# Optimization experiments

Hardware: AMD Instinct MI355X
Metric: run time of the kernel (lower is better)

## Reference

```python
import jax, jax.numpy as jnp
import numpy as np

N_NODES = 50000
N_EDGES = 500000
N_FEAT = 128
EMB_DIM = 1024
HIDDEN = 128
OUT_DIM = 10
VOCAB = 55049
N_GRAPHS = 64


def setup_inputs() -> dict:
    key = jax.random.key(0)
    ks = jax.random.split(key, 12)
    x = jax.random.normal(ks[0], (N_NODES, N_FEAT), dtype=jnp.float32)
    edge_weight = jax.random.uniform(ks[1], (N_EDGES,), dtype=jnp.float32)
    edge_index = jax.random.randint(ks[2], (2, N_EDGES), 0, N_NODES)
    batch = jnp.sort(jax.random.randint(ks[3], (N_NODES,), 0, N_GRAPHS))
    node_ids = jax.random.randint(ks[4], (N_NODES,), 0, VOCAB)
    emb_table = jax.random.normal(ks[5], (VOCAB, EMB_DIM), dtype=jnp.float32)
    d_in = N_FEAT + EMB_DIM
    W1 = jax.random.normal(ks[6], (d_in, HIDDEN), dtype=jnp.float32) / np.sqrt(d_in)
    b1 = jnp.zeros((HIDDEN,), dtype=jnp.float32)
    W2 = jax.random.normal(ks[7], (HIDDEN, HIDDEN), dtype=jnp.float32) / np.sqrt(HIDDEN)
    b2 = jnp.zeros((HIDDEN,), dtype=jnp.float32)
    fcW = jax.random.normal(ks[8], (HIDDEN, OUT_DIM), dtype=jnp.float32) / np.sqrt(HIDDEN)
    fcb = jnp.zeros((OUT_DIM,), dtype=jnp.float32)
    return dict(x=x, edge_weight=edge_weight, emb_table=emb_table, W1=W1, b1=b1,
                W2=W2, b2=b2, fcW=fcW, fcb=fcb,
                edge_index=edge_index, batch=batch, node_ids=node_ids)


def gcn_conv(x, edge_index, edge_weight, W, b, n_nodes):
    # PyG GCNConv: x' = D^{-1/2} (A + I) D^{-1/2} (x W) + b, self-loop weight = 1
    x = x @ W
    src, dst = edge_index[0], edge_index[1]
    loop = jnp.arange(n_nodes)
    src = jnp.concatenate([src, loop])
    dst = jnp.concatenate([dst, loop])
    ew = jnp.concatenate([edge_weight, jnp.ones((n_nodes,), x.dtype)])
    deg = jax.ops.segment_sum(ew, dst, num_segments=n_nodes)
    dinv = jnp.where(deg > 0, jax.lax.rsqrt(deg), 0.0)
    norm = dinv[src] * ew * dinv[dst]  # [E+N]
    msgs = norm[:, None] * x[src]      # [E+N, H] gather
    out = jax.ops.segment_sum(msgs, dst, num_segments=n_nodes)  # scatter-add
    return out + b


def reference(x, edge_weight, emb_table, W1, b1, W2, b2, fcW, fcb,
              edge_index, batch, node_ids):
    n = x.shape[0]
    h = jnp.concatenate([x, emb_table[node_ids]], axis=1)  # [N, F+E]
    h = jax.nn.relu(gcn_conv(h, edge_index, edge_weight, W1, b1, n))
    h = jax.nn.relu(gcn_conv(h, edge_index, edge_weight, W2, b2, n))
    # global mean pool per graph (dropout is identity in eval)
    sums = jax.ops.segment_sum(h, batch, num_segments=N_GRAPHS)
    counts = jax.ops.segment_sum(jnp.ones((n,), h.dtype), batch, num_segments=N_GRAPHS)
    pooled = sums / jnp.maximum(counts, 1.0)[:, None]
    return pooled @ fcW + fcb
```

## Files before the change

### kernel.cpp

```cpp
#include <hip/hip_runtime.h>
#include <hip/hip_bf16.h>

#define N_NODES 50000
#define N_EDGES 500000
#define N_FEAT 128
#define EMB_DIM 1024
#define HIDDEN 128
#define OUT_DIM 10
#define N_GRAPHS 64
#define NB_NODE 196

typedef __attribute__((ext_vector_type(8))) short short8;
typedef __attribute__((ext_vector_type(4))) float f32x4;

__device__ __forceinline__ unsigned short f2bf(float f) {
    unsigned int u = __float_as_uint(f);
    return (unsigned short)((u + 0x7fffu + ((u >> 16) & 1u)) >> 16);
}
__device__ __forceinline__ float bflo(unsigned int r) { return __uint_as_float(r << 16); }
__device__ __forceinline__ float bfhi(unsigned int r) { return __uint_as_float(r & 0xffff0000u); }
__device__ __forceinline__ unsigned int packbf(float lo, float hi) {
    return ((unsigned int)f2bf(hi) << 16) | f2bf(lo);
}

__global__ __launch_bounds__(256) void k_init(unsigned long long* __restrict__ dc,
                                              float* __restrict__ sums,
                                              float* __restrict__ counts) {
    int i = blockIdx.x * 256 + threadIdx.x;
    if (i < N_NODES) dc[i] = 0ULL;
    if (i < N_GRAPHS * HIDDEN) sums[i] = 0.0f;
    if (i < N_GRAPHS) counts[i] = 0.0f;
}

__global__ __launch_bounds__(256) void k_deg(const int* __restrict__ dst,
                                             const float* __restrict__ ew,
                                             unsigned long long* __restrict__ dc) {
    int e = blockIdx.x * 256 + threadIdx.x;
    if (e < N_EDGES) {
        unsigned int fx = (unsigned int)(ew[e] * 16777216.0f);
        atomicAdd(&dc[dst[e]], (1ULL << 32) | (unsigned long long)fx);
    }
}

__global__ __launch_bounds__(256) void k_scan1(const unsigned long long* __restrict__ dc,
                                               int* __restrict__ bsum) {
    __shared__ int wsum[4];
    int i = blockIdx.x * 256 + threadIdx.x;
    int v = (i < N_NODES) ? (int)((const uint2*)dc)[i].y : 0;
#pragma unroll
    for (int off = 32; off; off >>= 1) v += __shfl_down(v, off, 64);
    if ((threadIdx.x & 63) == 0) wsum[threadIdx.x >> 6] = v;
    __syncthreads();
    if (threadIdx.x == 0) bsum[blockIdx.x] = wsum[0] + wsum[1] + wsum[2] + wsum[3];
}

__global__ __launch_bounds__(256) void k_scan2(int* __restrict__ bsum) {
    __shared__ int sh[256];
    int t = threadIdx.x;
    int v = (t < NB_NODE) ? bsum[t] : 0;
    sh[t] = v;
    __syncthreads();
    for (int off = 1; off < 256; off <<= 1) {
        int add = (t >= off) ? sh[t - off] : 0;
        __syncthreads();
        sh[t] += add;
        __syncthreads();
    }
    if (t < NB_NODE) bsum[t] = sh[t] - v;
}

__global__ __launch_bounds__(256) void k_scan3(const unsigned long long* __restrict__ dc,
                                               const int* __restrict__ bofs,
                                               int* __restrict__ cursor,
                                               int* __restrict__ rowptr,
                                               float* __restrict__ dinv) {
    __shared__ int sh[256];
    const int t = threadIdx.x;
    const int i = blockIdx.x * 256 + t;
    uint2 d = (i < N_NODES) ? ((const uint2*)dc)[i] : make_uint2(0u, 0u);
    int v = (int)d.y;
    sh[t] = v;
    __syncthreads();
    for (int off = 1; off < 256; off <<= 1) {
        int add = (t >= off) ? sh[t - off] : 0;
        __syncthreads();
        sh[t] += add;
        __syncthreads();
    }
    int ex = sh[t] - v + bofs[blockIdx.x];
    if (i < N_NODES) {
        rowptr[i] = ex;
        cursor[i] = ex;
        float deg = 1.0f + (float)d.x * (1.0f / 16777216.0f);
        dinv[i] = 1.0f / sqrtf(deg);
    }
    if (i == 0) rowptr[N_NODES] = N_EDGES;
}

__global__ __launch_bounds__(256) void k_fill(const int* __restrict__ src,
                                              const int* __restrict__ dst,
                                              const float* __restrict__ ew,
                                              const float* __restrict__ dinv,
                                              int* __restrict__ cursor,
                                              int2* __restrict__ csr) {
    int e = blockIdx.x * 256 + threadIdx.x;
    if (e >= N_EDGES) return;
    int s = src[e], d = dst[e];
    int pos = atomicAdd(&cursor[d], 1);
    float norm = dinv[s] * ew[e] * dinv[d];
    csr[pos] = make_int2(s, __float_as_int(norm));
}

__device__ __forceinline__ void prep_one(const float* __restrict__ W,
                                         unsigned short* __restrict__ Wt,
                                         int K, int t) {
    int n = t & 127;
    int c = t >> 7;
    if (c * 16 >= K) return;
    short8 h0, h1;
#pragma unroll
    for (int i = 0; i < 16; i++) {
        unsigned short h = f2bf(W[(size_t)(c * 16 + i) * HIDDEN + n]);
        if (i < 8) h0[i] = (short)h;
        else       h1[i - 8] = (short)h;
    }
    size_t o = (size_t)n * K + c * 16;
    *(short8*)&Wt[o] = h0;
    *(short8*)&Wt[o + 8] = h1;
}

__global__ __launch_bounds__(256) void k_prep(const float* __restrict__ W1,
                                              unsigned short* __restrict__ Wt1,
                                              const float* __restrict__ W2,
                                              unsigned short* __restrict__ Wt2) {
    int b = blockIdx.x;
    if (b < 36) prep_one(W1, Wt1, N_FEAT + EMB_DIM, b * 256 + threadIdx.x);
    else        prep_one(W2, Wt2, HIDDEN, (b - 36) * 256 + threadIdx.x);
}

template <int MODE>
__global__ __launch_bounds__(256) void k_gemm(const float* __restrict__ X,
                                              const unsigned short* __restrict__ Xb,
                                              const float* __restrict__ EMB,
                                              const int* __restrict__ ids,
                                              const unsigned short* __restrict__ Wt,
                                              unsigned short* __restrict__ tbf, int K) {
    __shared__ unsigned short As[128][40];
    __shared__ unsigned short Bs[128][40];

    const int tid = threadIdx.x;
    const int lane = tid & 63;
    const int wv = tid >> 6;
    const int wm = wv >> 1, wn = wv & 1;
    const int fr = lane & 15;
    const int fq = lane >> 4;
    const int mBase = blockIdx.x * 128;

    const int aRow = tid >> 1;
    const int aOff = (tid & 1) * 16;
    const int m = mBase + aRow;
    const int mc = (m < N_NODES) ? m : (N_NODES - 1);
    int embRow = 0;
    if (MODE == 0) embRow = ids[mc];

    f32x4 acc[4][4];
#pragma unroll
    for (int i = 0; i < 4; i++)
#pragma unroll
        for (int j = 0; j < 4; j++) acc[i][j] = (f32x4){0.f, 0.f, 0.f, 0.f};

    float av[16];
    short8 axb0, axb1;
    short8 bh0, bh1;
    {
        if (MODE == 0) {
            const float* aptr = X + (size_t)mc * N_FEAT + aOff;
            *(float4*)&av[0]  = *(const float4*)(aptr);
            *(float4*)&av[4]  = *(const float4*)(aptr + 4);
            *(float4*)&av[8]  = *(const float4*)(aptr + 8);
            *(float4*)&av[12] = *(const float4*)(aptr + 12);
        } else {
            const unsigned short* aptr = Xb + (size_t)mc * HIDDEN + aOff;
            axb0 = *(const short8*)(aptr);
            axb1 = *(const short8*)(aptr + 8);
        }
        size_t bo = (size_t)aRow * K + aOff;
        bh0 = *(const short8*)&Wt[bo];
        bh1 = *(const short8*)&Wt[bo + 8];
    }

    for (int k0 = 0; k0 < K; k0 += 32) {
        short8 ah0, ah1;
        if (MODE == 0) {
#pragma unroll
            for (int i = 0; i < 16; i++) {
                unsigned short h = f2bf(av[i]);
                if (i < 8) ah0[i] = (short)h;
                else       ah1[i - 8] = (short)h;
            }
        } else {
            ah0 = axb0; ah1 = axb1;
        }
        *(short8*)&As[aRow][aOff] = ah0; *(short8*)&As[aRow][aOff + 8] = ah1;
        *(short8*)&Bs[aRow][aOff] = bh0; *(short8*)&Bs[aRow][aOff + 8] = bh1;
        __syncthreads();

        int k1 = k0 + 32;
        if (k1 < K) {
            if (MODE == 0) {
                const float* aptr = (k1 < N_FEAT)
                    ? X + (size_t)mc * N_FEAT + k1 + aOff
                    : EMB + (size_t)embRow * EMB_DIM + (k1 - N_FEAT) + aOff;
                *(float4*)&av[0]  = *(const float4*)(aptr);
                *(float4*)&av[4]  = *(const float4*)(aptr + 4);
                *(float4*)&av[8]  = *(const float4*)(aptr + 8);
                *(float4*)&av[12] = *(const float4*)(aptr + 12);
            } else {
                const unsigned short* aptr = Xb + (size_t)mc * HIDDEN + k1 + aOff;
                axb0 = *(const short8*)(aptr);
                axb1 = *(const short8*)(aptr + 8);
            }
            size_t bo = (size_t)aRow * K + k1 + aOff;
            bh0 = *(const short8*)&Wt[bo];
            bh1 = *(const short8*)&Wt[bo + 8];
        }

        short8 aF[4], bF[4];
#pragma unroll
        for (int i = 0; i < 4; i++) {
            aF[i] = *(const short8*)&As[wm * 64 + i * 16 + fr][fq * 8];
            bF[i] = *(const short8*)&Bs[wn * 64 + i * 16 + fr][fq * 8];
        }

#pragma unroll
        for (int i = 0; i < 4; i++)
#pragma unroll
            for (int j = 0; j < 4; j++)
                acc[i][j] = __builtin_amdgcn_mfma_f32_16x16x32_bf16(aF[i], bF[j], acc[i][j], 0, 0, 0);
        __syncthreads();
    }

#pragma unroll
    for (int i = 0; i < 4; i++) {
#pragma unroll
        for (int j = 0; j < 4; j++) {
            int gcol = wn * 64 + j * 16 + fr;
#pragma unroll
            for (int r = 0; r < 4; r++) {
                int grow = mBase + wm * 64 + i * 16 + fq * 4 + r;
                if (grow < N_NODES) tbf[(size_t)grow * HIDDEN + gcol] = f2bf(acc[i][j][r]);
            }
        }
    }
}

template <int POOL, int NWAVE>
__global__ __launch_bounds__(NWAVE * 64) void k_agg(const int2* __restrict__ csr,
                                                    const int* __restrict__ rowptr,
                                                    const float* __restrict__ dinv,
                                                    const unsigned short* __restrict__ tbf,
                                                    const float* __restrict__ bias,
                                                    const int* __restrict__ batch,
                                                    unsigned short* __restrict__ outb,
                                                    float* __restrict__ sums,
                                                    float* __restrict__ counts) {
    __shared__ float lsum[HIDDEN];
    __shared__ int lcnt;
    const int wv = threadIdx.x >> 6;
    const int lane = threadIdx.x & 63;
    const int grp = lane >> 4;
    const int q = lane & 15;
    const int gl = grp << 4;
    const int n = (blockIdx.x * NWAVE + wv) * 4 + grp;
    const uint4* t128 = (const uint4*)tbf;

    if (POOL) {
        if (threadIdx.x < HIDDEN) lsum[threadIdx.x] = 0.f;
        if (threadIdx.x == 0) lcnt = 0;
        __syncthreads();
    }

    float acc[8] = {};
    if (n < N_NODES) {
        const int beg = rowptr[n];
        const int end = rowptr[n + 1];
        const float di = dinv[n];
        const float wself = di * di;
        uint4 sr = t128[(size_t)n * 16 + q];
        float4 b0 = ((const float4*)bias)[q * 2];
        float4 b1 = ((const float4*)bias)[q * 2 + 1];
        acc[0] = fmaf(wself, bflo(sr.x), b0.x); acc[1] = fmaf(wself, bfhi(sr.x), b0.y);
        acc[2] = fmaf(wself, bflo(sr.y), b0.z); acc[3] = fmaf(wself, bfhi(sr.y), b0.w);
        acc[4] = fmaf(wself, bflo(sr.z), b1.x); acc[5] = fmaf(wself, bfhi(sr.z), b1.y);
        acc[6] = fmaf(wself, bflo(sr.w), b1.z); acc[7] = fmaf(wself, bfhi(sr.w), b1.w);

        for (int base = beg; base < end; base += 16) {
            int cnt = end - base; if (cnt > 16) cnt = 16;
            int2 ce = (q < cnt) ? csr[base + q] : make_int2(n, 0);
            for (int j = 0; j < cnt; j += 4) {
                int   s0 = __shfl(ce.x, gl + j);
                float w0 = __int_as_float(__shfl(ce.y, gl + j));
                int   s1 = __shfl(ce.x, gl + j + 1);
                float w1 = __int_as_float(__shfl(ce.y, gl + j + 1));
                int   s2 = __shfl(ce.x, gl + j + 2);
                float w2 = __int_as_float(__shfl(ce.y, gl + j + 2));
                int   s3 = __shfl(ce.x, gl + j + 3);
                float w3 = __int_as_float(__shfl(ce.y, gl + j + 3));
                uint4 r0 = t128[(size_t)s0 * 16 + q];
                uint4 r1 = t128[(size_t)s1 * 16 + q];
                uint4 r2 = t128[(size_t)s2 * 16 + q];
                uint4 r3 = t128[(size_t)s3 * 16 + q];
                acc[0] = fmaf(w0, bflo(r0.x), acc[0]); acc[1] = fmaf(w0, bfhi(r0.x), acc[1]);
                acc[2] = fmaf(w0, bflo(r0.y), acc[2]); acc[3] = fmaf(w0, bfhi(r0.y), acc[3]);
                acc[4] = fmaf(w0, bflo(r0.z), acc[4]); acc[5] = fmaf(w0, bfhi(r0.z), acc[5]);
                acc[6] = fmaf(w0, bflo(r0.w), acc[6]); acc[7] = fmaf(w0, bfhi(r0.w), acc[7]);
                acc[0] = fmaf(w1, bflo(r1.x), acc[0]); acc[1] = fmaf(w1, bfhi(r1.x), acc[1]);
                acc[2] = fmaf(w1, bflo(r1.y), acc[2]); acc[3] = fmaf(w1, bfhi(r1.y), acc[3]);
                acc[4] = fmaf(w1, bflo(r1.z), acc[4]); acc[5] = fmaf(w1, bfhi(r1.z), acc[5]);
                acc[6] = fmaf(w1, bflo(r1.w), acc[6]); acc[7] = fmaf(w1, bfhi(r1.w), acc[7]);
                acc[0] = fmaf(w2, bflo(r2.x), acc[0]); acc[1] = fmaf(w2, bfhi(r2.x), acc[1]);
                acc[2] = fmaf(w2, bflo(r2.y), acc[2]); acc[3] = fmaf(w2, bfhi(r2.y), acc[3]);
                acc[4] = fmaf(w2, bflo(r2.z), acc[4]); acc[5] = fmaf(w2, bfhi(r2.z), acc[5]);
                acc[6] = fmaf(w2, bflo(r2.w), acc[6]); acc[7] = fmaf(w2, bfhi(r2.w), acc[7]);
                acc[0] = fmaf(w3, bflo(r3.x), acc[0]); acc[1] = fmaf(w3, bfhi(r3.x), acc[1]);
                acc[2] = fmaf(w3, bflo(r3.y), acc[2]); acc[3] = fmaf(w3, bfhi(r3.y), acc[3]);
                acc[4] = fmaf(w3, bflo(r3.z), acc[4]); acc[5] = fmaf(w3, bfhi(r3.z), acc[5]);
                acc[6] = fmaf(w3, bflo(r3.w), acc[6]); acc[7] = fmaf(w3, bfhi(r3.w), acc[7]);
            }
        }
    }

    if (!POOL) {
        if (n < N_NODES) {
#pragma unroll
            for (int i = 0; i < 8; i++) acc[i] = fmaxf(acc[i], 0.f);
            uint4 o;
            o.x = packbf(acc[0], acc[1]);
            o.y = packbf(acc[2], acc[3]);
            o.z = packbf(acc[4], acc[5]);
            o.w = packbf(acc[6], acc[7]);
            ((uint4*)outb)[(size_t)n * 16 + q] = o;
        }
    } else {
        if (n < N_NODES) {
#pragma unroll
            for (int i = 0; i < 8; i++) acc[i] = fmaxf(acc[i], 0.f);
            int g = batch[n];
            int g0 = batch[blockIdx.x * NWAVE * 4];
            if (g == g0) {
#pragma unroll
                for (int i = 0; i < 8; i++) atomicAdd(&lsum[q * 8 + i], acc[i]);
                if (q == 0) atomicAdd(&lcnt, 1);
            } else {
#pragma unroll
                for (int i = 0; i < 8; i++) atomicAdd(&sums[g * HIDDEN + q * 8 + i], acc[i]);
                if (q == 0) atomicAdd(&counts[g], 1.0f);
            }
        }
        __syncthreads();
        int g0 = batch[blockIdx.x * NWAVE * 4];
        if (threadIdx.x < HIDDEN) atomicAdd(&sums[g0 * HIDDEN + threadIdx.x], lsum[threadIdx.x]);
        if (threadIdx.x == 0) atomicAdd(&counts[g0], (float)lcnt);
    }
}

__global__ __launch_bounds__(64) void k_final(const float* __restrict__ sums,
                                              const float* __restrict__ counts,
                                              const float* __restrict__ fcW,
                                              const float* __restrict__ fcb,
                                              float* __restrict__ out) {
    int g = blockIdx.x;
    int o = threadIdx.x;
    if (o >= OUT_DIM) return;
    float inv = 1.0f / fmaxf(counts[g], 1.0f);
    float acc = 0.f;
    for (int f = 0; f < HIDDEN; f++)
        acc = fmaf(sums[g * HIDDEN + f], fcW[f * OUT_DIM + o], acc);
    out[g * OUT_DIM + o] = acc * inv + fcb[o];
}

extern "C" void kernel_launch(void* const* d_in, const int* in_sizes, int n_in,
                              void* d_out, int out_size, void* d_ws, size_t ws_size,
                              hipStream_t stream) {
    const float* x      = (const float*)d_in[0];
    const float* ew     = (const float*)d_in[1];
    const float* emb    = (const float*)d_in[2];
    const float* W1     = (const float*)d_in[3];
    const float* b1     = (const float*)d_in[4];
    const float* W2     = (const float*)d_in[5];
    const float* b2     = (const float*)d_in[6];
    const float* fcW    = (const float*)d_in[7];
    const float* fcb    = (const float*)d_in[8];
    const int* edge_idx = (const int*)d_in[9];
    const int* batch    = (const int*)d_in[10];
    const int* node_ids = (const int*)d_in[11];
    float* out = (float*)d_out;

    const int* src = edge_idx;
    const int* dst = edge_idx + N_EDGES;

    float* ws     = (float*)d_ws;
    float* dinv   = ws;
    unsigned long long* dc = (unsigned long long*)(ws + 50048);
    int*   cursor = (int*)(ws + 150048);
    int*   rowptr = (int*)(ws + 200096);
    int*   bsum   = (int*)(ws + 250152);
    int2*  csr    = (int2*)(ws + 250408);
    unsigned short* tbf   = (unsigned short*)(ws + 1250408);
    unsigned short* out1b = (unsigned short*)(ws + 4450408);
    float* sums   = ws + 7650408;
    float* counts = sums + N_GRAPHS * HIDDEN;
    unsigned short* wt1 = (unsigned short*)(ws + 7658664);
    unsigned short* wt2 = (unsigned short*)(ws + 7732392);

    const int NB_EDGE = (N_EDGES + 255) / 256;
    const int NB_GEMM = (N_NODES + 127) / 128;
    const int NB_AGG  = (N_NODES + 15) / 16;
    const int K1 = N_FEAT + EMB_DIM;

    k_init <<<NB_NODE, 256, 0, stream>>>(dc, sums, counts);
    k_deg  <<<NB_EDGE, 256, 0, stream>>>(dst, ew, dc);
    k_scan1<<<NB_NODE, 256, 0, stream>>>(dc, bsum);
    k_scan2<<<1, 256, 0, stream>>>(bsum);
    k_scan3<<<NB_NODE, 256, 0, stream>>>(dc, bsum, cursor, rowptr, dinv);
    k_fill <<<NB_EDGE, 256, 0, stream>>>(src, dst, ew, dinv, cursor, csr);
    k_prep <<<40, 256, 0, stream>>>(W1, wt1, W2, wt2);

    k_gemm<0><<<NB_GEMM, 256, 0, stream>>>(x, nullptr, emb, node_ids, wt1, tbf, K1);
    k_agg<0, 4><<<NB_AGG, 256, 0, stream>>>(csr, rowptr, dinv, tbf, b1,
                                            batch, out1b, sums, counts);

    k_gemm<1><<<NB_GEMM, 256, 0, stream>>>(nullptr, out1b, nullptr, nullptr, wt2, tbf, HIDDEN);
    k_agg<1, 4><<<NB_AGG, 256, 0, stream>>>(csr, rowptr, dinv, tbf, b2,
                                            batch, nullptr, sums, counts);

    k_final<<<N_GRAPHS, 64, 0, stream>>>(sums, counts, fcW, fcb, out);
}
```

Before: 508.1 us.

## Merge small kernels and use hardware packed bf16 conversion

Folds the weight-prep work into the init kernel, drops the single-block scan2 by having every scan3 block redo the block-sum prefix scan, and moves the final FC into the last block of the second aggregation through a done-counter and threadfence. It also replaces the software round-to-nearest bf16 packing with the v_cvt_pk_bf16_f32 instruction in the GEMM A-tile conversion and the aggregation output. The goal is fewer kernel launches and fewer conversion ALU ops. In exchange each scan3 block repeats a small scan, and the final FC now runs serially inside a single block.

```diff
diff --git a/kernel.cpp b/kernel.cpp
--- a/kernel.cpp
+++ b/kernel.cpp
@@ -17,19 +17,48 @@
     unsigned int u = __float_as_uint(f);
     return (unsigned short)((u + 0x7fffu + ((u >> 16) & 1u)) >> 16);
 }
+__device__ __forceinline__ unsigned int cvtpk(float lo, float hi) {
+    unsigned int r;
+    asm volatile("v_cvt_pk_bf16_f32 %0, %1, %2" : "=v"(r) : "v"(lo), "v"(hi));
+    return r;
+}
 __device__ __forceinline__ float bflo(unsigned int r) { return __uint_as_float(r << 16); }
 __device__ __forceinline__ float bfhi(unsigned int r) { return __uint_as_float(r & 0xffff0000u); }
-__device__ __forceinline__ unsigned int packbf(float lo, float hi) {
-    return ((unsigned int)f2bf(hi) << 16) | f2bf(lo);
-}
-
-__global__ __launch_bounds__(256) void k_init(unsigned long long* __restrict__ dc,
-                                              float* __restrict__ sums,
-                                              float* __restrict__ counts) {
+
+__device__ __forceinline__ void prep_one(const float* __restrict__ W,
+                                         unsigned short* __restrict__ Wt,
+                                         int K, int t) {
+    int n = t & 127;
+    int c = t >> 7;
+    if (c * 16 >= K) return;
+    float v[16];
+#pragma unroll
+    for (int i = 0; i < 16; i++) v[i] = W[(size_t)(c * 16 + i) * HIDDEN + n];
+    uint4 o0, o1;
+    o0.x = cvtpk(v[0], v[1]);  o0.y = cvtpk(v[2], v[3]);
+    o0.z = cvtpk(v[4], v[5]);  o0.w = cvtpk(v[6], v[7]);
+    o1.x = cvtpk(v[8], v[9]);  o1.y = cvtpk(v[10], v[11]);
+    o1.z = cvtpk(v[12], v[13]); o1.w = cvtpk(v[14], v[15]);
+    size_t off = (size_t)n * K + c * 16;
+    *(uint4*)&Wt[off] = o0;
+    *(uint4*)&Wt[off + 8] = o1;
+}
+
+__global__ __launch_bounds__(256) void k_setup(unsigned long long* __restrict__ dc,
+                                               float* __restrict__ sums,
+                                               float* __restrict__ counts,
+                                               int* __restrict__ done,
+                                               const float* __restrict__ W1,
+                                               unsigned short* __restrict__ Wt1,
+                                               const float* __restrict__ W2,
+                                               unsigned short* __restrict__ Wt2) {
     int i = blockIdx.x * 256 + threadIdx.x;
     if (i < N_NODES) dc[i] = 0ULL;
     if (i < N_GRAPHS * HIDDEN) sums[i] = 0.0f;
     if (i < N_GRAPHS) counts[i] = 0.0f;
+    if (i == 0) *done = 0;
+    if (i < 9216) prep_one(W1, Wt1, N_FEAT + EMB_DIM, i);
+    else if (i < 10240) prep_one(W2, Wt2, HIDDEN, i - 9216);
 }
 
 __global__ __launch_bounds__(256) void k_deg(const int* __restrict__ dst,
@@ -54,29 +83,24 @@
     if (threadIdx.x == 0) bsum[blockIdx.x] = wsum[0] + wsum[1] + wsum[2] + wsum[3];
 }
 
-__global__ __launch_bounds__(256) void k_scan2(int* __restrict__ bsum) {
-    __shared__ int sh[256];
-    int t = threadIdx.x;
-    int v = (t < NB_NODE) ? bsum[t] : 0;
-    sh[t] = v;
-    __syncthreads();
-    for (int off = 1; off < 256; off <<= 1) {
-        int add = (t >= off) ? sh[t - off] : 0;
-        __syncthreads();
-        sh[t] += add;
-        __syncthreads();
-    }
-    if (t < NB_NODE) bsum[t] = sh[t] - v;
-}
-
 __global__ __launch_bounds__(256) void k_scan3(const unsigned long long* __restrict__ dc,
-                                               const int* __restrict__ bofs,
+                                               const int* __restrict__ bsum,
                                                int* __restrict__ cursor,
                                                int* __restrict__ rowptr,
                                                float* __restrict__ dinv) {
+    __shared__ int sb[256];
     __shared__ int sh[256];
     const int t = threadIdx.x;
     const int i = blockIdx.x * 256 + t;
+    sb[t] = (t < NB_NODE) ? bsum[t] : 0;
+    __syncthreads();
+    for (int off = 1; off < 256; off <<= 1) {
+        int add = (t >= off) ? sb[t - off] : 0;
+        __syncthreads();
+        sb[t] += add;
+        __syncthreads();
+    }
+    const int bofs = (blockIdx.x == 0) ? 0 : sb[blockIdx.x - 1];
     uint2 d = (i < N_NODES) ? ((const uint2*)dc)[i] : make_uint2(0u, 0u);
     int v = (int)d.y;
     sh[t] = v;
@@ -87,7 +111,7 @@
         sh[t] += add;
         __syncthreads();
     }
-    int ex = sh[t] - v + bofs[blockIdx.x];
+    int ex = sh[t] - v + bofs;
     if (i < N_NODES) {
         rowptr[i] = ex;
         cursor[i] = ex;
@@ -109,33 +133,6 @@
     int pos = atomicAdd(&cursor[d], 1);
     float norm = dinv[s] * ew[e] * dinv[d];
     csr[pos] = make_int2(s, __float_as_int(norm));
-}
-
-__device__ __forceinline__ void prep_one(const float* __restrict__ W,
-                                         unsigned short* __restrict__ Wt,
-                                         int K, int t) {
-    int n = t & 127;
-    int c = t >> 7;
-    if (c * 16 >= K) return;
-    short8 h0, h1;
-#pragma unroll
-    for (int i = 0; i < 16; i++) {
-        unsigned short h = f2bf(W[(size_t)(c * 16 + i) * HIDDEN + n]);
-        if (i < 8) h0[i] = (short)h;
-        else       h1[i - 8] = (short)h;
-    }
-    size_t o = (size_t)n * K + c * 16;
-    *(short8*)&Wt[o] = h0;
-    *(short8*)&Wt[o + 8] = h1;
-}
-
-__global__ __launch_bounds__(256) void k_prep(const float* __restrict__ W1,
-                                              unsigned short* __restrict__ Wt1,
-                                              const float* __restrict__ W2,
-                                              unsigned short* __restrict__ Wt2) {
-    int b = blockIdx.x;
-    if (b < 36) prep_one(W1, Wt1, N_FEAT + EMB_DIM, b * 256 + threadIdx.x);
-    else        prep_one(W2, Wt2, HIDDEN, (b - 36) * 256 + threadIdx.x);
 }
 
 template <int MODE>
@@ -190,18 +187,16 @@
     }
 
     for (int k0 = 0; k0 < K; k0 += 32) {
-        short8 ah0, ah1;
         if (MODE == 0) {
-#pragma unroll
-            for (int i = 0; i < 16; i++) {
-                unsigned short h = f2bf(av[i]);
-                if (i < 8) ah0[i] = (short)h;
-                else       ah1[i - 8] = (short)h;
-            }
+            uint4 a0, a1;
+            a0.x = cvtpk(av[0], av[1]);   a0.y = cvtpk(av[2], av[3]);
+            a0.z = cvtpk(av[4], av[5]);   a0.w = cvtpk(av[6], av[7]);
+            a1.x = cvtpk(av[8], av[9]);   a1.y = cvtpk(av[10], av[11]);
+            a1.z = cvtpk(av[12], av[13]); a1.w = cvtpk(av[14], av[15]);
+            *(uint4*)&As[aRow][aOff] = a0; *(uint4*)&As[aRow][aOff + 8] = a1;
         } else {
-            ah0 = axb0; ah1 = axb1;
-        }
-        *(short8*)&As[aRow][aOff] = ah0; *(short8*)&As[aRow][aOff + 8] = ah1;
+            *(short8*)&As[aRow][aOff] = axb0; *(short8*)&As[aRow][aOff + 8] = axb1;
+        }
         *(short8*)&Bs[aRow][aOff] = bh0; *(short8*)&Bs[aRow][aOff + 8] = bh1;
         __syncthreads();
 
@@ -263,7 +258,11 @@
                                                     const int* __restrict__ batch,
                                                     unsigned short* __restrict__ outb,
                                                     float* __restrict__ sums,
-                                                    float* __restrict__ counts) {
+                                                    float* __restrict__ counts,
+                                                    const float* __restrict__ fcW,
+                                                    const float* __restrict__ fcb,
+                                                    float* __restrict__ out,
+                                                    int* __restrict__ done) {
     __shared__ float lsum[HIDDEN];
     __shared__ int lcnt;
     const int wv = threadIdx.x >> 6;
@@ -335,10 +334,10 @@
 #pragma unroll
             for (int i = 0; i < 8; i++) acc[i] = fmaxf(acc[i], 0.f);
             uint4 o;
-            o.x = packbf(acc[0], acc[1]);
-            o.y = packbf(acc[2], acc[3]);
-            o.z = packbf(acc[4], acc[5]);
-            o.w = packbf(acc[6], acc[7]);
+            o.x = cvtpk(acc[0], acc[1]);
+            o.y = cvtpk(acc[2], acc[3]);
+            o.z = cvtpk(acc[4], acc[5]);
+            o.w = cvtpk(acc[6], acc[7]);
             ((uint4*)outb)[(size_t)n * 16 + q] = o;
         }
     } else {
@@ -361,22 +360,25 @@
         int g0 = batch[blockIdx.x * NWAVE * 4];
         if (threadIdx.x < HIDDEN) atomicAdd(&sums[g0 * HIDDEN + threadIdx.x], lsum[threadIdx.x]);
         if (threadIdx.x == 0) atomicAdd(&counts[g0], (float)lcnt);
-    }
-}
-
-__global__ __launch_bounds__(64) void k_final(const float* __restrict__ sums,
-                                              const float* __restrict__ counts,
-                                              const float* __restrict__ fcW,
-                                              const float* __restrict__ fcb,
-                                              float* __restrict__ out) {
-    int g = blockIdx.x;
-    int o = threadIdx.x;
-    if (o >= OUT_DIM) return;
-    float inv = 1.0f / fmaxf(counts[g], 1.0f);
-    float acc = 0.f;
-    for (int f = 0; f < HIDDEN; f++)
-        acc = fmaf(sums[g * HIDDEN + f], fcW[f * OUT_DIM + o], acc);
-    out[g * OUT_DIM + o] = acc * inv + fcb[o];
+
+        __threadfence();
+        __syncthreads();
+        __shared__ int lastFlag;
+        if (threadIdx.x == 0) lastFlag = (atomicAdd(done, 1) == (int)gridDim.x - 1);
+        __syncthreads();
+        if (lastFlag) {
+            __threadfence();
+            for (int t = threadIdx.x; t < N_GRAPHS * OUT_DIM; t += NWAVE * 64) {
+                int g = t / OUT_DIM, o = t - g * OUT_DIM;
+                float inv = 1.0f / fmaxf(counts[g], 1.0f);
+                float a = 0.f;
+#pragma unroll 8
+                for (int f = 0; f < HIDDEN; f++)
+                    a = fmaf(sums[g * HIDDEN + f], fcW[f * OUT_DIM + o], a);
+                out[g * OUT_DIM + o] = a * inv + fcb[o];
+            }
+        }
+    }
 }
 
 extern "C" void kernel_launch(void* const* d_in, const int* in_sizes, int n_in,
@@ -412,27 +414,24 @@
     float* counts = sums + N_GRAPHS * HIDDEN;
     unsigned short* wt1 = (unsigned short*)(ws + 7658664);
     unsigned short* wt2 = (unsigned short*)(ws + 7732392);
+    int*   done   = (int*)(ws + 7740584);
 
     const int NB_EDGE = (N_EDGES + 255) / 256;
     const int NB_GEMM = (N_NODES + 127) / 128;
     const int NB_AGG  = (N_NODES + 15) / 16;
     const int K1 = N_FEAT + EMB_DIM;
 
-    k_init <<<NB_NODE, 256, 0, stream>>>(dc, sums, counts);
+    k_setup<<<NB_NODE, 256, 0, stream>>>(dc, sums, counts, done, W1, wt1, W2, wt2);
     k_deg  <<<NB_EDGE, 256, 0, stream>>>(dst, ew, dc);
     k_scan1<<<NB_NODE, 256, 0, stream>>>(dc, bsum);
-    k_scan2<<<1, 256, 0, stream>>>(bsum);
     k_scan3<<<NB_NODE, 256, 0, stream>>>(dc, bsum, cursor, rowptr, dinv);
     k_fill <<<NB_EDGE, 256, 0, stream>>>(src, dst, ew, dinv, cursor, csr);
-    k_prep <<<40, 256, 0, stream>>>(W1, wt1, W2, wt2);
 
     k_gemm<0><<<NB_GEMM, 256, 0, stream>>>(x, nullptr, emb, node_ids, wt1, tbf, K1);
-    k_agg<0, 4><<<NB_AGG, 256, 0, stream>>>(csr, rowptr, dinv, tbf, b1,
-                                            batch, out1b, sums, counts);
+    k_agg<0, 4><<<NB_AGG, 256, 0, stream>>>(csr, rowptr, dinv, tbf, b1, batch, out1b,
+                                            sums, counts, nullptr, nullptr, nullptr, nullptr);
 
     k_gemm<1><<<NB_GEMM, 256, 0, stream>>>(nullptr, out1b, nullptr, nullptr, wt2, tbf, HIDDEN);
-    k_agg<1, 4><<<NB_AGG, 256, 0, stream>>>(csr, rowptr, dinv, tbf, b2,
-                                            batch, nullptr, sums, counts);
-
-    k_final<<<N_GRAPHS, 64, 0, stream>>>(sums, counts, fcW, fcb, out);
-}
+    k_agg<1, 4><<<NB_AGG, 256, 0, stream>>>(csr, rowptr, dinv, tbf, b2, batch, nullptr,
+                                            sums, counts, fcW, fcb, out, done);
+}
```

Measured after the change: 813.2 us. 60.1% more time.
